# Kernel tuning notes

Measured on AMD Instinct MI355X. Metric: run time of the kernel, lower is better.

The kernel has to match this reference:

```python
import jax, jax.numpy as jnp
import numpy as np

T, B, X, H1, H2 = 512, 256, 256, 256, 256


def setup_inputs() -> dict:
    key = jax.random.key(0)
    ks = jax.random.split(key, 9)
    s = 1.0 / np.sqrt(H1)
    return {
        "a_batch_of_seqs": jax.random.normal(ks[0], (T, B, X), dtype=jnp.float32),
        "initial_state_layer1": jnp.zeros((B, H1), dtype=jnp.float32),
        "initial_state_layer2": jnp.zeros((B, H2), dtype=jnp.float32),
        "W_ih1": jax.random.normal(ks[1], (H1, X), dtype=jnp.float32) * s,
        "W_hh1": jax.random.normal(ks[2], (H1, H1), dtype=jnp.float32) * s,
        "b_ih1": jax.random.normal(ks[3], (H1,), dtype=jnp.float32) * s,
        "b_hh1": jax.random.normal(ks[4], (H1,), dtype=jnp.float32) * s,
        "W_ih2": jax.random.normal(ks[5], (H2, H1), dtype=jnp.float32) * s,
        "W_hh2": jax.random.normal(ks[6], (H2, H2), dtype=jnp.float32) * s,
        "b_ih2": jax.random.normal(ks[7], (H2,), dtype=jnp.float32) * s,
        "b_hh2": jax.random.normal(ks[8], (H2,), dtype=jnp.float32) * s,
    }


def reference(a_batch_of_seqs, initial_state_layer1, initial_state_layer2,
              W_ih1, W_hh1, b_ih1, b_hh1, W_ih2, W_hh2, b_ih2, b_hh2):
    # Precompute input projections for both layers' input-to-hidden of layer1
    # (layer2's input depends on h1, so it stays inside the scan).
    x_proj = jnp.einsum('tbx,hx->tbh', a_batch_of_seqs, W_ih1) + b_ih1  # [T,B,H1]

    def step(carry, xp):
        h1, h2 = carry
        h1 = jnp.tanh(xp + h1 @ W_hh1.T + b_hh1)
        h2 = jnp.tanh(h1 @ W_ih2.T + b_ih2 + h2 @ W_hh2.T + b_hh2)
        return (h1, h2), h2

    (h1_f, h2_f), outputs = jax.lax.scan(step, (initial_state_layer1, initial_state_layer2), x_proj)
    return outputs, h1_f, h2_f
```

## Files before the change

### kernel.cpp

```cpp
#include <hip/hip_runtime.h>


#define TT 512
#define BB 256
#define HH 256
#define LSTR 280

typedef _Float16 f16;
typedef _Float16 f16x8 __attribute__((ext_vector_type(8)));
typedef float f32x4  __attribute__((ext_vector_type(4)));

__device__ inline float tanh_fast(float x) {
    float e = __expf(2.0f * x);
    return 1.0f - 2.0f * __builtin_amdgcn_rcpf(e + 1.0f);
}
__device__ inline void lds_barrier() {
    asm volatile("s_waitcnt lgkmcnt(0)\n\ts_barrier" ::: "memory");
}
__device__ inline f16x8 pack_wfragh(const float* __restrict__ wrow) {
    const float4* p = (const float4*)wrow;
    float4 v0 = p[0], v1 = p[1];
    f16x8 h;
    h[0] = (f16)v0.x; h[1] = (f16)v0.y; h[2] = (f16)v0.z; h[3] = (f16)v0.w;
    h[4] = (f16)v1.x; h[5] = (f16)v1.y; h[6] = (f16)v1.z; h[7] = (f16)v1.w;
    return h;
}
__device__ inline f32x4 mfma16h(f16x8 a, f16x8 b, f32x4 c) {
    return __builtin_amdgcn_mfma_f32_16x16x32_f16(a, b, c, 0, 0, 0);
}

__global__ __launch_bounds__(512, 2)
void proj_kernel(const float* __restrict__ Ain, const float* __restrict__ W,
                 const float* __restrict__ bias, float* __restrict__ Cout)
{
    __shared__ f16 lds_a[64 * LSTR];
    const int tid  = threadIdx.x;
    const int lane = tid & 63, wv = tid >> 6;
    const int quad = lane >> 4, l15 = lane & 15;
    const int n0   = wv * 32;

    f16x8 wh[2][8];
    float biasv[2];
#pragma unroll
    for (int nt = 0; nt < 2; ++nt) {
        int n = n0 + nt * 16 + l15;
        biasv[nt] = bias[n];
#pragma unroll
        for (int kc = 0; kc < 8; ++kc)
            wh[nt][kc] = pack_wfragh(W + (size_t)n * HH + kc * 32 + quad * 8);
    }

    for (int it = 0; it < 4; ++it) {
        const int m0 = (blockIdx.x * 4 + it) * 64;
#pragma unroll
        for (int j = 0; j < 8; ++j) {
            int c = tid + j * 512;
            int row = c >> 6, col4 = c & 63;
            float4 v = *(const float4*)(Ain + (size_t)(m0 + row) * HH + col4 * 4);
            f16 h0 = (f16)v.x, h1 = (f16)v.y, h2 = (f16)v.z, h3 = (f16)v.w;
            unsigned int p0 = (unsigned int)__builtin_bit_cast(unsigned short, h0) |
                              ((unsigned int)__builtin_bit_cast(unsigned short, h1) << 16);
            unsigned int p1 = (unsigned int)__builtin_bit_cast(unsigned short, h2) |
                              ((unsigned int)__builtin_bit_cast(unsigned short, h3) << 16);
            *(uint2*)&lds_a[row * LSTR + col4 * 4] = make_uint2(p0, p1);
        }
        __syncthreads();

        f32x4 acc[4][2];
#pragma unroll
        for (int mt = 0; mt < 4; ++mt)
#pragma unroll
            for (int nt = 0; nt < 2; ++nt)
                acc[mt][nt] = (f32x4){0.f, 0.f, 0.f, 0.f};

#pragma unroll
        for (int kc = 0; kc < 8; ++kc) {
            f16x8 ah[4];
#pragma unroll
            for (int mt = 0; mt < 4; ++mt)
                ah[mt] = *(const f16x8*)&lds_a[(mt * 16 + l15) * LSTR + kc * 32 + quad * 8];
#pragma unroll
            for (int mt = 0; mt < 4; ++mt)
#pragma unroll
                for (int nt = 0; nt < 2; ++nt)
                    acc[mt][nt] = mfma16h(ah[mt], wh[nt][kc], acc[mt][nt]);
        }

#pragma unroll
        for (int mt = 0; mt < 4; ++mt)
#pragma unroll
            for (int nt = 0; nt < 2; ++nt)
#pragma unroll
                for (int r = 0; r < 4; ++r) {
                    int row = m0 + mt * 16 + quad * 4 + r;
                    int col = n0 + nt * 16 + l15;
                    Cout[(size_t)row * HH + col] = acc[mt][nt][r] + biasv[nt];
                }
        __syncthreads();
    }
}

__global__ __launch_bounds__(512, 2)
void fused_scan_kernel(float* __restrict__ xu,
                       const float* __restrict__ Whh1,
                       const float* __restrict__ bhh1,
                       const float* __restrict__ Wih2,
                       const float* __restrict__ Whh2,
                       const float* __restrict__ bih2,
                       const float* __restrict__ bhh2,
                       const float* __restrict__ h10,
                       const float* __restrict__ h20,
                       float* __restrict__ h1f,
                       float* __restrict__ h2f)
{
    __shared__ f16 hs1[2][16 * LSTR];
    __shared__ f16 hs2[2][16 * LSTR];
    const int tid  = threadIdx.x;
    const int lane = tid & 63, wv = tid >> 6;
    const int quad = lane >> 4, l15 = lane & 15;
    const int m0   = blockIdx.x * 16;
    const int n0   = wv * 32;

    f16x8 w1[2][8], w2[2][8], w3[2][8];
    float b1v[2], b2v[2];
#pragma unroll
    for (int nt = 0; nt < 2; ++nt) {
        int n = n0 + nt * 16 + l15;
        b1v[nt] = bhh1[n];
        b2v[nt] = bih2[n] + bhh2[n];
#pragma unroll
        for (int kc = 0; kc < 8; ++kc) {
            w1[nt][kc] = pack_wfragh(Whh1 + (size_t)n * HH + kc * 32 + quad * 8);
            w2[nt][kc] = pack_wfragh(Wih2 + (size_t)n * HH + kc * 32 + quad * 8);
            w3[nt][kc] = pack_wfragh(Whh2 + (size_t)n * HH + kc * 32 + quad * 8);
        }
    }
#pragma unroll
    for (int j = 0; j < 8; ++j) {
        int idx = tid + j * 512;
        int row = idx >> 8, col = idx & 255;
        hs1[0][row * LSTR + col] = (f16)h10[(size_t)(m0 + row) * HH + col];
        hs2[0][row * LSTR + col] = (f16)h20[(size_t)(m0 + row) * HH + col];
    }
    __syncthreads();

    const int colb = n0 + l15;
    const int rowb = quad * 4;

    for (int t = 0; t < TT; ++t) {
        const int cur = t & 1, nxt = (t + 1) & 1;
        const size_t base = ((size_t)t * BB + m0) * HH;

        float xc[2][4];
#pragma unroll
        for (int nt = 0; nt < 2; ++nt)
#pragma unroll
            for (int r = 0; r < 4; ++r)
                xc[nt][r] = xu[base + (size_t)(rowb + r) * HH + colb + nt * 16];

        f32x4 acc1[2] = {(f32x4){0.f,0.f,0.f,0.f}, (f32x4){0.f,0.f,0.f,0.f}};
        f32x4 acc3[2] = {(f32x4){0.f,0.f,0.f,0.f}, (f32x4){0.f,0.f,0.f,0.f}};
#pragma unroll
        for (int kc = 0; kc < 8; ++kc) {
            f16x8 a1 = *(const f16x8*)&hs1[cur][l15 * LSTR + kc * 32 + quad * 8];
            f16x8 a3 = *(const f16x8*)&hs2[cur][l15 * LSTR + kc * 32 + quad * 8];
#pragma unroll
            for (int nt = 0; nt < 2; ++nt) {
                acc1[nt] = mfma16h(a1, w1[nt][kc], acc1[nt]);
                acc3[nt] = mfma16h(a3, w3[nt][kc], acc3[nt]);
            }
        }

#pragma unroll
        for (int nt = 0; nt < 2; ++nt)
#pragma unroll
            for (int r = 0; r < 4; ++r) {
                float pre = acc1[nt][r] + xc[nt][r] + b1v[nt];
                float h   = tanh_fast(pre);
                hs1[nxt][(rowb + r) * LSTR + colb + nt * 16] = (f16)h;
                if (t == TT - 1)
                    h1f[(size_t)(m0 + rowb + r) * HH + colb + nt * 16] = h;
            }
        lds_barrier();

        f32x4 acc2[2] = {(f32x4){0.f,0.f,0.f,0.f}, (f32x4){0.f,0.f,0.f,0.f}};
#pragma unroll
        for (int kc = 0; kc < 8; ++kc) {
            f16x8 a2 = *(const f16x8*)&hs1[nxt][l15 * LSTR + kc * 32 + quad * 8];
#pragma unroll
            for (int nt = 0; nt < 2; ++nt)
                acc2[nt] = mfma16h(a2, w2[nt][kc], acc2[nt]);
        }

#pragma unroll
        for (int nt = 0; nt < 2; ++nt)
#pragma unroll
            for (int r = 0; r < 4; ++r) {
                float pre = acc2[nt][r] + acc3[nt][r] + b2v[nt];
                float h   = tanh_fast(pre);
                hs2[nxt][(rowb + r) * LSTR + colb + nt * 16] = (f16)h;
                xu[base + (size_t)(rowb + r) * HH + colb + nt * 16] = h;
                if (t == TT - 1)
                    h2f[(size_t)(m0 + rowb + r) * HH + colb + nt * 16] = h;
            }
        lds_barrier();
    }
}

extern "C" void kernel_launch(void* const* d_in, const int* in_sizes, int n_in,
                              void* d_out, int out_size, void* d_ws, size_t ws_size,
                              hipStream_t stream)
{
    const float* A     = (const float*)d_in[0];
    const float* is1   = (const float*)d_in[1];
    const float* is2   = (const float*)d_in[2];
    const float* W_ih1 = (const float*)d_in[3];
    const float* W_hh1 = (const float*)d_in[4];
    const float* b_ih1 = (const float*)d_in[5];
    const float* b_hh1 = (const float*)d_in[6];
    const float* W_ih2 = (const float*)d_in[7];
    const float* W_hh2 = (const float*)d_in[8];
    const float* b_ih2 = (const float*)d_in[9];
    const float* b_hh2 = (const float*)d_in[10];

    float* out = (float*)d_out;
    const size_t OUT0 = (size_t)TT * BB * HH;
    float* x1  = out;
    float* h1f = out + OUT0;
    float* h2f = out + OUT0 + (size_t)BB * HH;
    (void)d_ws; (void)ws_size;

    proj_kernel<<<dim3(512), dim3(512), 0, stream>>>(A, W_ih1, b_ih1, x1);
    fused_scan_kernel<<<dim3(16), dim3(512), 0, stream>>>(
        x1, W_hh1, b_hh1, W_ih2, W_hh2, b_ih2, b_hh2, is1, is2, h1f, h2f);
}
```

Baseline: 1.166 ms.

## Skew layer-1 and layer-2 recurrences so each step needs one barrier

The two-layer scan is software-pipelined. A prologue computes h1 for step 0, and each loop iteration then computes h2[t] from h1[t] and h2[t-1] together with h1[t+1] from h1[t] and x[t+1]. This removes one LDS barrier per timestep and lets all three MFMA chains issue back to back, shortening the serial dependency per step. The cost is one extra, discarded h1 update on the last iteration, slightly more register pressure, and the final h1 being written one iteration early.

```diff
diff --git a/kernel.cpp b/kernel.cpp
--- a/kernel.cpp
+++ b/kernel.cpp
@@ -139,7 +139,7 @@
     for (int j = 0; j < 8; ++j) {
         int idx = tid + j * 512;
         int row = idx >> 8, col = idx & 255;
-        hs1[0][row * LSTR + col] = (f16)h10[(size_t)(m0 + row) * HH + col];
+        hs1[1][row * LSTR + col] = (f16)h10[(size_t)(m0 + row) * HH + col];
         hs2[0][row * LSTR + col] = (f16)h20[(size_t)(m0 + row) * HH + col];
     }
     __syncthreads();
@@ -147,27 +147,57 @@
     const int colb = n0 + l15;
     const int rowb = quad * 4;
 
-    for (int t = 0; t < TT; ++t) {
-        const int cur = t & 1, nxt = (t + 1) & 1;
-        const size_t base = ((size_t)t * BB + m0) * HH;
-
-        float xc[2][4];
+    {
+        float x0[2][4];
 #pragma unroll
         for (int nt = 0; nt < 2; ++nt)
 #pragma unroll
             for (int r = 0; r < 4; ++r)
-                xc[nt][r] = xu[base + (size_t)(rowb + r) * HH + colb + nt * 16];
+                x0[nt][r] = xu[(size_t)(m0 + rowb + r) * HH + colb + nt * 16];
+
+        f32x4 p[2] = {(f32x4){0.f,0.f,0.f,0.f}, (f32x4){0.f,0.f,0.f,0.f}};
+#pragma unroll
+        for (int kc = 0; kc < 8; ++kc) {
+            f16x8 a = *(const f16x8*)&hs1[1][l15 * LSTR + kc * 32 + quad * 8];
+#pragma unroll
+            for (int nt = 0; nt < 2; ++nt)
+                p[nt] = mfma16h(a, w1[nt][kc], p[nt]);
+        }
+#pragma unroll
+        for (int nt = 0; nt < 2; ++nt)
+#pragma unroll
+            for (int r = 0; r < 4; ++r) {
+                float h = tanh_fast(p[nt][r] + x0[nt][r] + b1v[nt]);
+                hs1[0][(rowb + r) * LSTR + colb + nt * 16] = (f16)h;
+            }
+        __syncthreads();
+    }
+
+    for (int i = 0; i < TT; ++i) {
+        const int cur = i & 1, nxt = cur ^ 1;
+        const size_t basew = ((size_t)i * BB + m0) * HH;
+        const int ir = (i + 1 < TT) ? (i + 1) : i;
+        const size_t baser = ((size_t)ir * BB + m0) * HH;
+
+        float xn[2][4];
+#pragma unroll
+        for (int nt = 0; nt < 2; ++nt)
+#pragma unroll
+            for (int r = 0; r < 4; ++r)
+                xn[nt][r] = xu[baser + (size_t)(rowb + r) * HH + colb + nt * 16];
 
         f32x4 acc1[2] = {(f32x4){0.f,0.f,0.f,0.f}, (f32x4){0.f,0.f,0.f,0.f}};
+        f32x4 acc2[2] = {(f32x4){0.f,0.f,0.f,0.f}, (f32x4){0.f,0.f,0.f,0.f}};
         f32x4 acc3[2] = {(f32x4){0.f,0.f,0.f,0.f}, (f32x4){0.f,0.f,0.f,0.f}};
 #pragma unroll
         for (int kc = 0; kc < 8; ++kc) {
             f16x8 a1 = *(const f16x8*)&hs1[cur][l15 * LSTR + kc * 32 + quad * 8];
-            f16x8 a3 = *(const f16x8*)&hs2[cur][l15 * LSTR + kc * 32 + quad * 8];
+            f16x8 a2 = *(const f16x8*)&hs2[cur][l15 * LSTR + kc * 32 + quad * 8];
 #pragma unroll
             for (int nt = 0; nt < 2; ++nt) {
+                acc2[nt] = mfma16h(a1, w2[nt][kc], acc2[nt]);
                 acc1[nt] = mfma16h(a1, w1[nt][kc], acc1[nt]);
-                acc3[nt] = mfma16h(a3, w3[nt][kc], acc3[nt]);
+                acc3[nt] = mfma16h(a2, w3[nt][kc], acc3[nt]);
             }
         }
 
@@ -175,33 +205,15 @@
         for (int nt = 0; nt < 2; ++nt)
 #pragma unroll
             for (int r = 0; r < 4; ++r) {
-                float pre = acc1[nt][r] + xc[nt][r] + b1v[nt];
-                float h   = tanh_fast(pre);
-                hs1[nxt][(rowb + r) * LSTR + colb + nt * 16] = (f16)h;
-                if (t == TT - 1)
-                    h1f[(size_t)(m0 + rowb + r) * HH + colb + nt * 16] = h;
-            }
-        lds_barrier();
-
-        f32x4 acc2[2] = {(f32x4){0.f,0.f,0.f,0.f}, (f32x4){0.f,0.f,0.f,0.f}};
-#pragma unroll
-        for (int kc = 0; kc < 8; ++kc) {
-            f16x8 a2 = *(const f16x8*)&hs1[nxt][l15 * LSTR + kc * 32 + quad * 8];
-#pragma unroll
-            for (int nt = 0; nt < 2; ++nt)
-                acc2[nt] = mfma16h(a2, w2[nt][kc], acc2[nt]);
-        }
-
-#pragma unroll
-        for (int nt = 0; nt < 2; ++nt)
-#pragma unroll
-            for (int r = 0; r < 4; ++r) {
-                float pre = acc2[nt][r] + acc3[nt][r] + b2v[nt];
-                float h   = tanh_fast(pre);
-                hs2[nxt][(rowb + r) * LSTR + colb + nt * 16] = (f16)h;
-                xu[base + (size_t)(rowb + r) * HH + colb + nt * 16] = h;
-                if (t == TT - 1)
-                    h2f[(size_t)(m0 + rowb + r) * HH + colb + nt * 16] = h;
+                const int row = rowb + r, col = colb + nt * 16;
+                float h2v = tanh_fast(acc2[nt][r] + acc3[nt][r] + b2v[nt]);
+                hs2[nxt][row * LSTR + col] = (f16)h2v;
+                xu[basew + (size_t)row * HH + col] = h2v;
+                if (i == TT - 1) h2f[(size_t)(m0 + row) * HH + col] = h2v;
+
+                float h1v = tanh_fast(acc1[nt][r] + xn[nt][r] + b1v[nt]);
+                hs1[nxt][row * LSTR + col] = (f16)h1v;
+                if (i == TT - 2) h1f[(size_t)(m0 + row) * HH + col] = h1v;
             }
         lds_barrier();
     }
```

Measured after the change: 1.070 ms. 8.2% less time.
